# Optimization experiments

Hardware: AMD Instinct MI355X
Metric: run time of the kernel (lower is better)

Reference implementation:

```python
import jax, jax.numpy as jnp
import numpy as np

NUM_CLASSES = 5  # config['training']['num_classes_per_task']


def _conv(x, w, b):
    # x: [N,C,H,W], w: [O,I,kh,kw] (torch OIHW), valid padding, stride 1
    y = jax.lax.conv_general_dilated(
        x, w, window_strides=(1, 1), padding='VALID',
        dimension_numbers=('NCHW', 'OIHW', 'NCHW'))
    return y + b[None, :, None, None]


def _maxpool2(x):
    return jax.lax.reduce_window(x, -jnp.inf, jax.lax.max,
                                 (1, 1, 2, 2), (1, 1, 2, 2), 'VALID')


def _lenet(x, c1w, c1b, c2w, c2b, f1w, f1b, f2w, f2b, f3w, f3b):
    h = _maxpool2(jax.nn.relu(_conv(x, c1w, c1b)))   # [N,6,14,14]
    h = _maxpool2(jax.nn.relu(_conv(h, c2w, c2b)))   # [N,16,5,5]
    h = h.reshape(h.shape[0], -1)                     # [N,400]
    h = jax.nn.relu(h @ f1w.T + f1b)                  # [N,120]
    h = jax.nn.relu(h @ f2w.T + f2b)                  # [N,84]
    return h @ f3w.T + f3b                            # [N,64] embeddings


def setup_inputs() -> dict:
    key = jax.random.key(0)
    ks = jax.random.split(key, 7)
    def w(k, shape, fan_in):
        return jax.random.normal(k, shape, jnp.float32) * (1.0 / np.sqrt(fan_in))
    return {
        'x': jax.random.normal(ks[0], (20480, 3, 32, 32), jnp.float32),
        'c1w': w(ks[1], (6, 3, 5, 5), 3 * 25), 'c1b': jnp.zeros((6,), jnp.float32),
        'c2w': w(ks[2], (16, 6, 5, 5), 6 * 25), 'c2b': jnp.zeros((16,), jnp.float32),
        'f1w': w(ks[3], (120, 400), 400), 'f1b': jnp.zeros((120,), jnp.float32),
        'f2w': w(ks[4], (84, 120), 120), 'f2b': jnp.zeros((84,), jnp.float32),
        'f3w': w(ks[5], (64, 84), 84), 'f3b': jnp.zeros((64,), jnp.float32),
    }


def reference(x, c1w, c1b, c2w, c2b, f1w, f1b, f2w, f2b, f3w, f3b):
    emb = _lenet(x, c1w, c1b, c2w, c2b, f1w, f1b, f2w, f2b, f3w, f3b)  # [N,64]
    # prototypes = embeddings.sum() / num_classes  (scalar, as in source)
    proto = emb.sum() / NUM_CLASSES
    result = jax.nn.softmax(emb, axis=1)
    # sqrt((result - proto)^2) elementwise == |result - proto|; the python
    # per-sample list-comprehension just rebuilds this same [N,64] tensor.
    return jnp.sqrt(jnp.square(result - proto))
```

## Files before the change

### kernel.cpp

```cpp
#include <hip/hip_runtime.h>
#include <math.h>

typedef __attribute__((ext_vector_type(8))) short short8;
typedef __attribute__((ext_vector_type(4))) float f32x4;
typedef __attribute__((ext_vector_type(4))) unsigned short us4v;

__device__ __forceinline__ unsigned short f2bf(float f) {
    unsigned u = __float_as_uint(f);
    return (unsigned short)((u + 0x7FFFu + ((u >> 16) & 1u)) >> 16);
}
__device__ __forceinline__ unsigned cvtpk(float lo, float hi) {
    unsigned r;
    asm("v_cvt_pk_bf16_f32 %0, %1, %2" : "=v"(r) : "v"(lo), "v"(hi));
    return r;
}
__device__ __forceinline__ unsigned short f2bf1(float v) {
    return (unsigned short)(cvtpk(v, 0.f) & 0xffffu);
}
__device__ __forceinline__ float fmax_x8(float v) {
    int s = __builtin_amdgcn_mov_dpp(__float_as_int(v), 0x128, 0xf, 0xf, true);
    return fmaxf(v, __int_as_float(s));
}

#define C1T_SS 3464
#define C1_RS 36
#define P1R 1176

__global__ __launch_bounds__(256, 3) void conv12_mfma(
    const float* __restrict__ x,
    const unsigned short* __restrict__ c1wf, const float* __restrict__ c1b,
    const unsigned short* __restrict__ c2wf, const float* __restrict__ c2b,
    unsigned short* __restrict__ P2)
{
    __shared__ __align__(16) unsigned short img[2 * C1T_SS];
    __shared__ __align__(16) unsigned short p1s[16 * P1R + 16];
    const int t = threadIdx.x;
    const int lane = t & 63, w = t >> 6;
    const int grp = lane >> 4, c = lane & 15;
    const int smp = c >> 3, q = c & 7;

    if (t < 192) {
        int s = t / 96, rr = t - s * 96;
        *(uint2*)&img[s * C1T_SS + rr * C1_RS + 32] = make_uint2(0u, 0u);
    }
    if (t < 2) {
        *(uint4*)&img[t * C1T_SS + 3456] = make_uint4(0u, 0u, 0u, 0u);
        *(uint4*)&p1s[16 * P1R + t * 8] = make_uint4(0u, 0u, 0u, 0u);
    }

    short8 wf1[5][4];
#pragma unroll
    for (int s = 0; s < 5; s++)
#pragma unroll
        for (int off = 0; off < 4; off++)
            wf1[s][off] = *(const short8*)&c1wf[(((s * 4 + off) * 4 + grp) * 16 + c) * 8];
    int ciA[5], kpA[5];
#pragma unroll
    for (int s = 0; s < 5; s++) {
        int b = s * 4 + grp; if (b > 17) b = 17;
        ciA[s] = b / 6; kpA[s] = b % 6;
    }
    const float bias1 = (c < 6) ? c1b[c] : 0.f;

    const float4* xs4 = (const float4*)(x + (size_t)blockIdx.x * 49152);
    float4 r[6];

#pragma unroll
    for (int k = 0; k < 6; k++) r[k] = xs4[k * 256 + t];

    for (int st = 0; st < 8; st++) {
#pragma unroll
        for (int k = 0; k < 6; k++) {
            int f = k * 256 + t;
            int s = (f >= 768) ? 1 : 0;
            int w4 = f - s * 768;
            int ci = w4 >> 8, rem = w4 & 255, y = rem >> 3, xq = rem & 7;
            uint2 pk = make_uint2(cvtpk(r[k].x, r[k].y), cvtpk(r[k].z, r[k].w));
            *(uint2*)&img[s * C1T_SS + (ci * 32 + y) * C1_RS + xq * 4] = pk;
        }
        __syncthreads();

        if (st < 7) {
#pragma unroll
            for (int k = 0; k < 6; k++) r[k] = xs4[(st + 1) * 1536 + k * 256 + t];
        }

        for (int py = w; py < 14; py += 4) {
            f32x4 a00 = {0.f,0.f,0.f,0.f}, a01 = a00, a10 = a00, a11 = a00;
#pragma unroll
            for (int s = 0; s < 5; s++) {
                int e = smp * C1T_SS + (ciA[s] * 32 + py * 2 + kpA[s]) * C1_RS + q * 4;
                union { us4v h[2]; short8 v; } af;
                af.h[0] = *(const us4v*)&img[e];
                af.h[1] = *(const us4v*)&img[e + 4];
                a00 = __builtin_amdgcn_mfma_f32_16x16x32_bf16(af.v, wf1[s][0], a00, 0, 0, 0);
                a01 = __builtin_amdgcn_mfma_f32_16x16x32_bf16(af.v, wf1[s][1], a01, 0, 0, 0);
                a10 = __builtin_amdgcn_mfma_f32_16x16x32_bf16(af.v, wf1[s][2], a10, 0, 0, 0);
                a11 = __builtin_amdgcn_mfma_f32_16x16x32_bf16(af.v, wf1[s][3], a11, 0, 0, 0);
            }
            f32x4 pe2, po2;
#pragma unroll
            for (int i = 0; i < 4; i++) {
                pe2[i] = fmax_x8(fmaxf(a00[i], a01[i]));
                po2[i] = fmax_x8(fmaxf(a10[i], a11[i]));
            }
            if (c < 6) {
#pragma unroll
                for (int i = 0; i < 4; i++) {
                    int m = grp * 4 + i;
                    int qo = m & 7;
                    if (qo < 7) {
                        int sm = m >> 3;
                        float v0 = fmaxf(pe2[i] + bias1, 0.f);
                        float v1 = fmaxf(po2[i] + bias1, 0.f);
                        *(unsigned*)&p1s[(2 * st + sm) * P1R + (c * 14 + py) * 14 + qo * 2]
                            = cvtpk(v0, v1);
                    }
                }
            }
        }
        __syncthreads();
    }

    short8 wf2[8][2];
#pragma unroll
    for (int s = 0; s < 8; s++)
#pragma unroll
        for (int off = 0; off < 2; off++)
            wf2[s][off] = *(const short8*)&c2wf[(((s * 2 + off) * 4 + grp) * 16 + c) * 8];
    int ciB[8], kyB[8];
#pragma unroll
    for (int s = 0; s < 8; s++) {
        int b = s * 4 + grp; if (b > 29) b = 29;
        ciB[s] = b / 5; kyB[s] = b % 5;
    }
    const float bias2 = c2b[c];

    unsigned pkbuf[7][2];
#pragma unroll
    for (int j = 0; j < 7; j++) {
        const int item = w + j * 4;
        if (item < 25) {
            const int py = item / 5, px = item % 5;
            f32x4 a00 = {0.f,0.f,0.f,0.f}, a01 = a00, a10 = a00, a11 = a00;
#pragma unroll
            for (int s = 0; s < 8; s++) {
                int rbase = ciB[s] * 14 + kyB[s] + py * 2;
#pragma unroll
                for (int yo = 0; yo < 2; yo++) {
                    int e = c * P1R + (rbase + yo) * 14 + px * 2;
                    union { unsigned u[4]; short8 v; } af;
                    af.u[0] = *(const unsigned*)&p1s[e];
                    af.u[1] = *(const unsigned*)&p1s[e + 2];
                    af.u[2] = *(const unsigned*)&p1s[e + 4];
                    af.u[3] = *(const unsigned*)&p1s[e + 6];
                    if (yo == 0) {
                        a00 = __builtin_amdgcn_mfma_f32_16x16x32_bf16(af.v, wf2[s][0], a00, 0, 0, 0);
                        a01 = __builtin_amdgcn_mfma_f32_16x16x32_bf16(af.v, wf2[s][1], a01, 0, 0, 0);
                    } else {
                        a10 = __builtin_amdgcn_mfma_f32_16x16x32_bf16(af.v, wf2[s][0], a10, 0, 0, 0);
                        a11 = __builtin_amdgcn_mfma_f32_16x16x32_bf16(af.v, wf2[s][1], a11, 0, 0, 0);
                    }
                }
            }
            float v0 = fmaxf(fmaxf(fmaxf(a00[0], a01[0]), fmaxf(a10[0], a11[0])) + bias2, 0.f);
            float v1 = fmaxf(fmaxf(fmaxf(a00[1], a01[1]), fmaxf(a10[1], a11[1])) + bias2, 0.f);
            float v2 = fmaxf(fmaxf(fmaxf(a00[2], a01[2]), fmaxf(a10[2], a11[2])) + bias2, 0.f);
            float v3 = fmaxf(fmaxf(fmaxf(a00[3], a01[3]), fmaxf(a10[3], a11[3])) + bias2, 0.f);
            pkbuf[j][0] = cvtpk(v0, v1);
            pkbuf[j][1] = cvtpk(v2, v3);
        }
    }
    __syncthreads();

    unsigned short* p2t = p1s;
#pragma unroll
    for (int j = 0; j < 7; j++) {
        const int item = w + j * 4;
        if (item < 25) {
#pragma unroll
            for (int i = 0; i < 4; i++) {
                unsigned v = pkbuf[j][i >> 1] >> ((i & 1) * 16);
                p2t[(grp * 4 + i) * 400 + c * 25 + item] = (unsigned short)v;
            }
        }
    }
    __syncthreads();

    uint4* dst = (uint4*)(P2 + (size_t)blockIdx.x * 6400);
    const uint4* srcT = (const uint4*)p2t;
    for (int e = t; e < 800; e += 256) dst[e] = srcT[e];
}

__global__ __launch_bounds__(256) void prep_weights(
    const float* __restrict__ c1w, const float* __restrict__ c2w,
    const float* __restrict__ f1w, const float* __restrict__ f2w,
    const float* __restrict__ f3w,
    unsigned short* __restrict__ wb1, unsigned short* __restrict__ wb2,
    unsigned short* __restrict__ wb3,
    unsigned short* __restrict__ c1wf, unsigned short* __restrict__ c2wf)
{
    const int t0 = blockIdx.x * 256 + threadIdx.x;
    const int stride = gridDim.x * 256;
    for (int i = t0; i < 128 * 416; i += stride) {
        int o = i / 416, k = i % 416;
        wb1[i] = f2bf((o < 120 && k < 400) ? f1w[o * 400 + k] : 0.f);
    }
    for (int i = t0; i < 96 * 128; i += stride) {
        int o = i / 128, k = i % 128;
        wb2[i] = f2bf((o < 84 && k < 120) ? f2w[o * 120 + k] : 0.f);
    }
    for (int i = t0; i < 64 * 96; i += stride) {
        int o = i / 96, k = i % 96;
        wb3[i] = f2bf((k < 84) ? f3w[o * 84 + k] : 0.f);
    }
    for (int i = t0; i < 10240; i += stride) {
        int j = i & 7, c = (i >> 3) & 15, grp = (i >> 7) & 3;
        int off = (i >> 9) & 3, s = i >> 11;
        int b = s * 4 + grp;
        int ci = b / 6, kp = b % 6;
        int kx = j - off;
        float v = 0.f;
        if (b < 18 && kx >= 0 && kx <= 4) {
            if (c < 6 && kp <= 4)
                v = c1w[c * 75 + ci * 25 + kp * 5 + kx];
            else if (c >= 8 && c < 14 && kp >= 1)
                v = c1w[(c - 8) * 75 + ci * 25 + (kp - 1) * 5 + kx];
        }
        c1wf[i] = f2bf(v);
    }
    for (int i = t0; i < 8192; i += stride) {
        int j = i & 7, c = (i >> 3) & 15, grp = (i >> 7) & 3;
        int off = (i >> 9) & 1, s = i >> 10;
        int b = s * 4 + grp;
        int kx = j - off;
        float v = 0.f;
        if (b < 30 && kx >= 0 && kx <= 4) {
            int ci = b / 5, ky = b % 5;
            v = c2w[c * 150 + ci * 25 + ky * 5 + kx];
        }
        c2wf[i] = f2bf(v);
    }
}

#define FCS 32
#define P2S 424
#define A1S 136
#define A2S 104

__global__ __launch_bounds__(256, 3) void fc_mfma(
    const unsigned short* __restrict__ P2,
    const unsigned short* __restrict__ wb1, const float* __restrict__ f1b,
    const unsigned short* __restrict__ wb2, const float* __restrict__ f2b,
    const unsigned short* __restrict__ wb3, const float* __restrict__ f3b,
    float* __restrict__ emb, float* __restrict__ part)
{
    __shared__ __align__(16) unsigned short p2s[FCS * P2S];
    __shared__ __align__(16) unsigned short a1s[FCS * A1S];
    __shared__ __align__(16) unsigned short a2s[FCS * A2S];
    __shared__ float rsum[4];
    const int t = threadIdx.x, lane = t & 63, w = t >> 6;
    const int grp = lane >> 4, c = lane & 15;

    if (t < 64) {
        int s = t >> 1, h = t & 1;
        *(uint4*)&p2s[s * P2S + 400 + h * 8] = make_uint4(0u, 0u, 0u, 0u);
    }
    const uint4* src = (const uint4*)(P2 + (size_t)blockIdx.x * FCS * 400);
    for (int i = t; i < FCS * 50; i += 256) {
        int s = i / 50, k8 = i % 50;
        *(uint4*)&p2s[s * P2S + k8 * 8] = src[i];
    }
    __syncthreads();

    const int m = w & 1;
    const int arow = m * 16 + c;

    {
        const int n0 = (w >> 1) * 4;
        f32x4 acc[4] = {{0.f,0.f,0.f,0.f},{0.f,0.f,0.f,0.f},{0.f,0.f,0.f,0.f},{0.f,0.f,0.f,0.f}};
        const int sb = arow * P2S;
#pragma unroll
        for (int ks = 0; ks < 13; ks++) {
            short8 a = *(const short8*)&p2s[sb + ks * 32 + grp * 8];
#pragma unroll
            for (int j = 0; j < 4; j++) {
                int o = (n0 + j) * 16 + c;
                short8 b = *(const short8*)&wb1[o * 416 + ks * 32 + grp * 8];
                acc[j] = __builtin_amdgcn_mfma_f32_16x16x32_bf16(a, b, acc[j], 0, 0, 0);
            }
        }
#pragma unroll
        for (int j = 0; j < 4; j++) {
            int o = (n0 + j) * 16 + c;
            float bias = (o < 120) ? f1b[o] : 0.f;
#pragma unroll
            for (int i = 0; i < 4; i++) {
                int s = m * 16 + grp * 4 + i;
                a1s[s * A1S + o] = f2bf1(fmaxf(acc[j][i] + bias, 0.f));
            }
        }
    }
    __syncthreads();

    {
        const int n0 = (w >> 1) * 3;
        f32x4 acc[3] = {{0.f,0.f,0.f,0.f},{0.f,0.f,0.f,0.f},{0.f,0.f,0.f,0.f}};
        const int sb = arow * A1S;
#pragma unroll
        for (int ks = 0; ks < 4; ks++) {
            short8 a = *(const short8*)&a1s[sb + ks * 32 + grp * 8];
#pragma unroll
            for (int j = 0; j < 3; j++) {
                int o = (n0 + j) * 16 + c;
                short8 b = *(const short8*)&wb2[o * 128 + ks * 32 + grp * 8];
                acc[j] = __builtin_amdgcn_mfma_f32_16x16x32_bf16(a, b, acc[j], 0, 0, 0);
            }
        }
#pragma unroll
        for (int j = 0; j < 3; j++) {
            int o = (n0 + j) * 16 + c;
            float bias = (o < 84) ? f2b[o] : 0.f;
#pragma unroll
            for (int i = 0; i < 4; i++) {
                int s = m * 16 + grp * 4 + i;
                a2s[s * A2S + o] = f2bf1(fmaxf(acc[j][i] + bias, 0.f));
            }
        }
    }
    __syncthreads();

    {
        const int n0 = (w >> 1) * 2;
        f32x4 acc[2] = {{0.f,0.f,0.f,0.f},{0.f,0.f,0.f,0.f}};
        const int sb = arow * A2S;
#pragma unroll
        for (int ks = 0; ks < 3; ks++) {
            short8 a = *(const short8*)&a2s[sb + ks * 32 + grp * 8];
#pragma unroll
            for (int j = 0; j < 2; j++) {
                int o = (n0 + j) * 16 + c;
                short8 b = *(const short8*)&wb3[o * 96 + ks * 32 + grp * 8];
                acc[j] = __builtin_amdgcn_mfma_f32_16x16x32_bf16(a, b, acc[j], 0, 0, 0);
            }
        }
        float psum = 0.f;
#pragma unroll
        for (int j = 0; j < 2; j++) {
            int o = (n0 + j) * 16 + c;
            float bias = f3b[o];
#pragma unroll
            for (int i = 0; i < 4; i++) {
                int s = m * 16 + grp * 4 + i;
                float v = acc[j][i] + bias;
                emb[((size_t)blockIdx.x * FCS + s) * 64 + o] = v;
                psum += v;
            }
        }
#pragma unroll
        for (int off = 32; off; off >>= 1) psum += __shfl_xor(psum, off);
        if (lane == 0) rsum[w] = psum;
        __syncthreads();
        if (t == 0) part[blockIdx.x] = (rsum[0] + rsum[1]) + (rsum[2] + rsum[3]);
    }
}

__global__ __launch_bounds__(256) void softmax_abs(float* __restrict__ io,
                                                   const float* __restrict__ part) {
    const int lane = threadIdx.x & 63;
    const int row = (blockIdx.x << 2) + (threadIdx.x >> 6);
    float e = io[(size_t)row * 64 + lane];
    float ps = 0.f;
#pragma unroll
    for (int k = 0; k < 10; k++) ps += part[k * 64 + lane];
#pragma unroll
    for (int off = 32; off; off >>= 1) ps += __shfl_xor(ps, off);
    const float proto = ps / 5.0f;
    float m = e;
#pragma unroll
    for (int off = 32; off; off >>= 1) m = fmaxf(m, __shfl_xor(m, off));
    float p = expf(e - m);
    float s = p;
#pragma unroll
    for (int off = 32; off; off >>= 1) s += __shfl_xor(s, off);
    io[(size_t)row * 64 + lane] = fabsf(p / s - proto);
}

extern "C" void kernel_launch(void* const* d_in, const int* in_sizes, int n_in,
                              void* d_out, int out_size, void* d_ws, size_t ws_size,
                              hipStream_t stream) {
    const float* x   = (const float*)d_in[0];
    const float* c1w = (const float*)d_in[1];
    const float* c1b = (const float*)d_in[2];
    const float* c2w = (const float*)d_in[3];
    const float* c2b = (const float*)d_in[4];
    const float* f1w = (const float*)d_in[5];
    const float* f1b = (const float*)d_in[6];
    const float* f2w = (const float*)d_in[7];
    const float* f2b = (const float*)d_in[8];
    const float* f3w = (const float*)d_in[9];
    const float* f3b = (const float*)d_in[10];
    float* out = (float*)d_out;

    const int N = in_sizes[0] / 3072;
    const size_t p2_bytes = (size_t)N * 400 * 2;
    unsigned short* P2 = (unsigned short*)d_ws;
    char* tail = (char*)d_ws + p2_bytes;
    float* part  = (float*)tail;
    unsigned short* wb1  = (unsigned short*)(tail + 4096);
    unsigned short* wb2  = wb1 + 128 * 416;
    unsigned short* wb3  = wb2 + 96 * 128;
    unsigned short* c1wf = wb3 + 64 * 96;
    unsigned short* c2wf = c1wf + 10240;

    prep_weights<<<64, 256, 0, stream>>>(c1w, c2w, f1w, f2w, f3w,
                                         wb1, wb2, wb3, c1wf, c2wf);
    conv12_mfma<<<N / 16, 256, 0, stream>>>(x, c1wf, c1b, c2wf, c2b, P2);
    fc_mfma<<<N / 32, 256, 0, stream>>>(P2, wb1, f1b, wb2, f2b, wb3, f3b, out, part);
    softmax_abs<<<N / 4, 256, 0, stream>>>(out, part);
}
```

Before: 106.7 us.

## Fuse FC layers into conv kernel to drop P2 intermediate round-trip

```diff
diff --git a/kernel.cpp b/kernel.cpp
--- a/kernel.cpp
+++ b/kernel.cpp
@@ -25,15 +25,22 @@
 #define C1T_SS 3464
 #define C1_RS 36
 #define P1R 1176
-
-__global__ __launch_bounds__(256, 3) void conv12_mfma(
+#define P2S 424
+#define A1S 136
+#define A2S 104
+
+__global__ __launch_bounds__(256, 3) void conv12fc_mfma(
     const float* __restrict__ x,
     const unsigned short* __restrict__ c1wf, const float* __restrict__ c1b,
     const unsigned short* __restrict__ c2wf, const float* __restrict__ c2b,
-    unsigned short* __restrict__ P2)
+    const unsigned short* __restrict__ wb1, const float* __restrict__ f1b,
+    const unsigned short* __restrict__ wb2, const float* __restrict__ f2b,
+    const unsigned short* __restrict__ wb3, const float* __restrict__ f3b,
+    float* __restrict__ emb, float* __restrict__ part)
 {
     __shared__ __align__(16) unsigned short img[2 * C1T_SS];
     __shared__ __align__(16) unsigned short p1s[16 * P1R + 16];
+    __shared__ float rsum[4];
     const int t = threadIdx.x;
     const int lane = t & 63, w = t >> 6;
     const int grp = lane >> 4, c = lane & 15;
@@ -181,15 +188,98 @@
 #pragma unroll
             for (int i = 0; i < 4; i++) {
                 unsigned v = pkbuf[j][i >> 1] >> ((i & 1) * 16);
-                p2t[(grp * 4 + i) * 400 + c * 25 + item] = (unsigned short)v;
-            }
-        }
+                p2t[(grp * 4 + i) * P2S + c * 25 + item] = (unsigned short)v;
+            }
+        }
+    }
+    if (t < 32) {
+        int s = t >> 1, h = t & 1;
+        *(uint4*)&p2t[s * P2S + 400 + h * 8] = make_uint4(0u, 0u, 0u, 0u);
     }
     __syncthreads();
 
-    uint4* dst = (uint4*)(P2 + (size_t)blockIdx.x * 6400);
-    const uint4* srcT = (const uint4*)p2t;
-    for (int e = t; e < 800; e += 256) dst[e] = srcT[e];
+    unsigned short* a1s = img;
+    unsigned short* a2s = img + 16 * A1S;
+    {
+        f32x4 acc[2] = {{0.f,0.f,0.f,0.f},{0.f,0.f,0.f,0.f}};
+        const int sb = c * P2S;
+#pragma unroll
+        for (int ks = 0; ks < 13; ks++) {
+            short8 a = *(const short8*)&p2t[sb + ks * 32 + grp * 8];
+#pragma unroll
+            for (int j = 0; j < 2; j++) {
+                int o = (w + 4 * j) * 16 + c;
+                short8 b = *(const short8*)&wb1[o * 416 + ks * 32 + grp * 8];
+                acc[j] = __builtin_amdgcn_mfma_f32_16x16x32_bf16(a, b, acc[j], 0, 0, 0);
+            }
+        }
+        __syncthreads();
+#pragma unroll
+        for (int j = 0; j < 2; j++) {
+            int o = (w + 4 * j) * 16 + c;
+            float bias = (o < 120) ? f1b[o] : 0.f;
+#pragma unroll
+            for (int i = 0; i < 4; i++)
+                a1s[(grp * 4 + i) * A1S + o] = f2bf1(fmaxf(acc[j][i] + bias, 0.f));
+        }
+    }
+    __syncthreads();
+
+    {
+        f32x4 acc[2] = {{0.f,0.f,0.f,0.f},{0.f,0.f,0.f,0.f}};
+        const int sb = c * A1S;
+#pragma unroll
+        for (int ks = 0; ks < 4; ks++) {
+            short8 a = *(const short8*)&a1s[sb + ks * 32 + grp * 8];
+#pragma unroll
+            for (int j = 0; j < 2; j++) {
+                int nt = w + 4 * j;
+                if (nt < 6) {
+                    int o = nt * 16 + c;
+                    short8 b = *(const short8*)&wb2[o * 128 + ks * 32 + grp * 8];
+                    acc[j] = __builtin_amdgcn_mfma_f32_16x16x32_bf16(a, b, acc[j], 0, 0, 0);
+                }
+            }
+        }
+        __syncthreads();
+#pragma unroll
+        for (int j = 0; j < 2; j++) {
+            int nt = w + 4 * j;
+            if (nt < 6) {
+                int o = nt * 16 + c;
+                float bias = (o < 84) ? f2b[o] : 0.f;
+#pragma unroll
+                for (int i = 0; i < 4; i++)
+                    a2s[(grp * 4 + i) * A2S + o] = f2bf1(fmaxf(acc[j][i] + bias, 0.f));
+            }
+        }
+    }
+    __syncthreads();
+
+    {
+        f32x4 acc = {0.f,0.f,0.f,0.f};
+        const int sb = c * A2S;
+        const int o = w * 16 + c;
+#pragma unroll
+        for (int ks = 0; ks < 3; ks++) {
+            short8 a = *(const short8*)&a2s[sb + ks * 32 + grp * 8];
+            short8 b = *(const short8*)&wb3[o * 96 + ks * 32 + grp * 8];
+            acc = __builtin_amdgcn_mfma_f32_16x16x32_bf16(a, b, acc, 0, 0, 0);
+        }
+        const float bias = f3b[o];
+        float psum = 0.f;
+#pragma unroll
+        for (int i = 0; i < 4; i++) {
+            float v = acc[i] + bias;
+            emb[((size_t)blockIdx.x * 16 + grp * 4 + i) * 64 + o] = v;
+            psum += v;
+        }
+#pragma unroll
+        for (int off = 32; off; off >>= 1) psum += __shfl_xor(psum, off);
+        if (lane == 0) rsum[w] = psum;
+        __syncthreads();
+        if (t == 0) part[blockIdx.x] = (rsum[0] + rsum[1]) + (rsum[2] + rsum[3]);
+    }
 }
 
 __global__ __launch_bounds__(256) void prep_weights(
@@ -243,128 +333,6 @@
     }
 }
 
-#define FCS 32
-#define P2S 424
-#define A1S 136
-#define A2S 104
-
-__global__ __launch_bounds__(256, 3) void fc_mfma(
-    const unsigned short* __restrict__ P2,
-    const unsigned short* __restrict__ wb1, const float* __restrict__ f1b,
-    const unsigned short* __restrict__ wb2, const float* __restrict__ f2b,
-    const unsigned short* __restrict__ wb3, const float* __restrict__ f3b,
-    float* __restrict__ emb, float* __restrict__ part)
-{
-    __shared__ __align__(16) unsigned short p2s[FCS * P2S];
-    __shared__ __align__(16) unsigned short a1s[FCS * A1S];
-    __shared__ __align__(16) unsigned short a2s[FCS * A2S];
-    __shared__ float rsum[4];
-    const int t = threadIdx.x, lane = t & 63, w = t >> 6;
-    const int grp = lane >> 4, c = lane & 15;
-
-    if (t < 64) {
-        int s = t >> 1, h = t & 1;
-        *(uint4*)&p2s[s * P2S + 400 + h * 8] = make_uint4(0u, 0u, 0u, 0u);
-    }
-    const uint4* src = (const uint4*)(P2 + (size_t)blockIdx.x * FCS * 400);
-    for (int i = t; i < FCS * 50; i += 256) {
-        int s = i / 50, k8 = i % 50;
-        *(uint4*)&p2s[s * P2S + k8 * 8] = src[i];
-    }
-    __syncthreads();
-
-    const int m = w & 1;
-    const int arow = m * 16 + c;
-
-    {
-        const int n0 = (w >> 1) * 4;
-        f32x4 acc[4] = {{0.f,0.f,0.f,0.f},{0.f,0.f,0.f,0.f},{0.f,0.f,0.f,0.f},{0.f,0.f,0.f,0.f}};
-        const int sb = arow * P2S;
-#pragma unroll
-        for (int ks = 0; ks < 13; ks++) {
-            short8 a = *(const short8*)&p2s[sb + ks * 32 + grp * 8];
-#pragma unroll
-            for (int j = 0; j < 4; j++) {
-                int o = (n0 + j) * 16 + c;
-                short8 b = *(const short8*)&wb1[o * 416 + ks * 32 + grp * 8];
-                acc[j] = __builtin_amdgcn_mfma_f32_16x16x32_bf16(a, b, acc[j], 0, 0, 0);
-            }
-        }
-#pragma unroll
-        for (int j = 0; j < 4; j++) {
-            int o = (n0 + j) * 16 + c;
-            float bias = (o < 120) ? f1b[o] : 0.f;
-#pragma unroll
-            for (int i = 0; i < 4; i++) {
-                int s = m * 16 + grp * 4 + i;
-                a1s[s * A1S + o] = f2bf1(fmaxf(acc[j][i] + bias, 0.f));
-            }
-        }
-    }
-    __syncthreads();
-
-    {
-        const int n0 = (w >> 1) * 3;
-        f32x4 acc[3] = {{0.f,0.f,0.f,0.f},{0.f,0.f,0.f,0.f},{0.f,0.f,0.f,0.f}};
-        const int sb = arow * A1S;
-#pragma unroll
-        for (int ks = 0; ks < 4; ks++) {
-            short8 a = *(const short8*)&a1s[sb + ks * 32 + grp * 8];
-#pragma unroll
-            for (int j = 0; j < 3; j++) {
-                int o = (n0 + j) * 16 + c;
-                short8 b = *(const short8*)&wb2[o * 128 + ks * 32 + grp * 8];
-                acc[j] = __builtin_amdgcn_mfma_f32_16x16x32_bf16(a, b, acc[j], 0, 0, 0);
-            }
-        }
-#pragma unroll
-        for (int j = 0; j < 3; j++) {
-            int o = (n0 + j) * 16 + c;
-            float bias = (o < 84) ? f2b[o] : 0.f;
-#pragma unroll
-            for (int i = 0; i < 4; i++) {
-                int s = m * 16 + grp * 4 + i;
-                a2s[s * A2S + o] = f2bf1(fmaxf(acc[j][i] + bias, 0.f));
-            }
-        }
-    }
-    __syncthreads();
-
-    {
-        const int n0 = (w >> 1) * 2;
-        f32x4 acc[2] = {{0.f,0.f,0.f,0.f},{0.f,0.f,0.f,0.f}};
-        const int sb = arow * A2S;
-#pragma unroll
-        for (int ks = 0; ks < 3; ks++) {
-            short8 a = *(const short8*)&a2s[sb + ks * 32 + grp * 8];
-#pragma unroll
-            for (int j = 0; j < 2; j++) {
-                int o = (n0 + j) * 16 + c;
-                short8 b = *(const short8*)&wb3[o * 96 + ks * 32 + grp * 8];
-                acc[j] = __builtin_amdgcn_mfma_f32_16x16x32_bf16(a, b, acc[j], 0, 0, 0);
-            }
-        }
-        float psum = 0.f;
-#pragma unroll
-        for (int j = 0; j < 2; j++) {
-            int o = (n0 + j) * 16 + c;
-            float bias = f3b[o];
-#pragma unroll
-            for (int i = 0; i < 4; i++) {
-                int s = m * 16 + grp * 4 + i;
-                float v = acc[j][i] + bias;
-                emb[((size_t)blockIdx.x * FCS + s) * 64 + o] = v;
-                psum += v;
-            }
-        }
-#pragma unroll
-        for (int off = 32; off; off >>= 1) psum += __shfl_xor(psum, off);
-        if (lane == 0) rsum[w] = psum;
-        __syncthreads();
-        if (t == 0) part[blockIdx.x] = (rsum[0] + rsum[1]) + (rsum[2] + rsum[3]);
-    }
-}
-
 __global__ __launch_bounds__(256) void softmax_abs(float* __restrict__ io,
                                                    const float* __restrict__ part) {
     const int lane = threadIdx.x & 63;
@@ -372,7 +340,7 @@
     float e = io[(size_t)row * 64 + lane];
     float ps = 0.f;
 #pragma unroll
-    for (int k = 0; k < 10; k++) ps += part[k * 64 + lane];
+    for (int k = 0; k < 20; k++) ps += part[k * 64 + lane];
 #pragma unroll
     for (int off = 32; off; off >>= 1) ps += __shfl_xor(ps, off);
     const float proto = ps / 5.0f;
@@ -403,11 +371,8 @@
     float* out = (float*)d_out;
 
     const int N = in_sizes[0] / 3072;
-    const size_t p2_bytes = (size_t)N * 400 * 2;
-    unsigned short* P2 = (unsigned short*)d_ws;
-    char* tail = (char*)d_ws + p2_bytes;
-    float* part  = (float*)tail;
-    unsigned short* wb1  = (unsigned short*)(tail + 4096);
+    float* part = (float*)d_ws;
+    unsigned short* wb1  = (unsigned short*)((char*)d_ws + 8192);
     unsigned short* wb2  = wb1 + 128 * 416;
     unsigned short* wb3  = wb2 + 96 * 128;
     unsigned short* c1wf = wb3 + 64 * 96;
@@ -415,7 +380,8 @@
 
     prep_weights<<<64, 256, 0, stream>>>(c1w, c2w, f1w, f2w, f3w,
                                          wb1, wb2, wb3, c1wf, c2wf);
-    conv12_mfma<<<N / 16, 256, 0, stream>>>(x, c1wf, c1b, c2wf, c2b, P2);
-    fc_mfma<<<N / 32, 256, 0, stream>>>(P2, wb1, f1b, wb2, f2b, wb3, f3b, out, part);
+    conv12fc_mfma<<<N / 16, 256, 0, stream>>>(x, c1wf, c1b, c2wf, c2b,
+                                              wb1, f1b, wb2, f2b, wb3, f3b,
+                                              out, part);
     softmax_abs<<<N / 4, 256, 0, stream>>>(out, part);
 }
```

Result: faster. 94.26 us, median of 2 (-11.7%).
